# Optimization experiments

Measured on AMD Instinct MI355X. Metric: run time of the kernel, lower is better.

## Reference

```python
import jax, jax.numpy as jnp
import numpy as np

TOKEN_BITS = 10
CODEBOOK_SIZE = 2 ** TOKEN_BITS  # 1024
COMMITMENT_COST = 0.25
ENTROPY_LOSS_WEIGHT = 0.1
ENTROPY_TEMPERATURE = 0.01
ENTROPY_GAMMA = 1.0
EPS = 1e-5


def _make_codebook():
    bits_to_indices = (2 ** jnp.arange(TOKEN_BITS)).astype(jnp.int32)          # [c]
    all_codes = jnp.arange(CODEBOOK_SIZE, dtype=jnp.int32)                      # [n]
    bits = ((all_codes[:, None] & bits_to_indices) != 0).astype(jnp.float32)    # [n, c]
    codebook = bits * 2.0 - 1.0                                                 # [n, c] in {-1,+1}
    return bits_to_indices, codebook


def setup_inputs() -> dict:
    key = jax.random.key(0)
    z = jax.random.normal(key, (16, TOKEN_BITS, 64, 64), dtype=jnp.float32)
    return {"z": z}


def reference(z):
    bits_to_indices, codebook = _make_codebook()

    # b c h w -> b h w c
    zp = jnp.transpose(z, (0, 2, 3, 1)).astype(jnp.float32)

    # sign quantization to {-1, +1}
    sign_mask = zp > 0.0
    z_q = jnp.where(sign_mask, 1.0, -1.0).astype(jnp.float32)

    # pack sign bits into codebook indices
    min_encoding_indices = jnp.sum(sign_mask.astype(jnp.int32) * bits_to_indices, axis=-1)  # [b,h,w]

    # commitment loss (stop-grad on the quantized target)
    commitment_loss = COMMITMENT_COST * jnp.mean((jax.lax.stop_gradient(z_q) - zp) ** 2)

    # entropy loss: logits = -d = 2 * z . codebook^T, softened by temperature
    logits = 2.0 * jnp.einsum('bhwc,nc->bhwn', zp, codebook)  # [b,h,w,n]
    log_probs = jax.nn.log_softmax(logits / ENTROPY_TEMPERATURE, axis=-1)
    probs = jnp.exp(log_probs)
    per_sample_entropy = jnp.mean(-jnp.sum(probs * log_probs, axis=-1))
    avg_probs = jnp.mean(probs, axis=(0, 1, 2))  # [n]
    avg_entropy = ENTROPY_GAMMA * (-jnp.sum(avg_probs * jnp.log(avg_probs + EPS)))
    entropy_loss = ENTROPY_LOSS_WEIGHT * (per_sample_entropy - avg_entropy)

    loss = commitment_loss + entropy_loss

    # straight-through estimator
    z_quantized = zp + jax.lax.stop_gradient(z_q - zp)
    # b h w c -> b c h w
    z_quantized = jnp.transpose(z_quantized, (0, 3, 1, 2))

    return z_quantized, loss, per_sample_entropy, min_encoding_indices
```

## Files before the change

### kernel.cpp

```cpp
#include <hip/hip_runtime.h>

#define NCH    10
#define NCODE  1024
#define NLOC   65536
#define NZ     655360
#define GRID   256
#define THR    256
#define NHIST  4
#define POISON_INT (-1431655766)

__device__ __forceinline__ float wave_reduce_sum(float v) {
#pragma unroll
    for (int off = 32; off > 0; off >>= 1)
        v += __shfl_down(v, off, 64);
    return v;
}

__global__ __launch_bounds__(THR) void lfq_fused(
    const float* __restrict__ z, float* __restrict__ out,
    float* __restrict__ wsH, float* __restrict__ wsC, float* __restrict__ wsE,
    int* __restrict__ wsN)
{
    __shared__ float sR[NCH][THR];
    __shared__ unsigned short sM[NCH][THR];
    __shared__ float red[8];
    __shared__ int lastFlag;

    const int tid  = threadIdx.x;
    const int loc  = blockIdx.x * THR + tid;
    const int b    = loc >> 12;
    const int base = b * (NCH * 4096) + (loc & 4095);
    float* hist = wsH + (blockIdx.x & (NHIST - 1)) * NCODE;

    float commit = 0.f, ent = 0.f, pstar = 1.f;
    int idx = 0, k = 0;
#pragma unroll
    for (int c = 0; c < NCH; ++c) {
        float zc = z[base + c * 4096];
        bool bit = zc > 0.f;
        float s = bit ? 1.f : -1.f;
        out[base + c * 4096] = s;
        if (bit) idx |= (1 << c);
        float d = s - zc;
        commit += d * d;
        float a = fabsf(zc) * 400.f;
        if (a < 23.0f) {
            float e = __expf(-a);
            float inv = 1.f / (1.f + e);
            ent += __logf(1.f + e) + a * e * inv;
            pstar *= inv;
            sR[k][tid] = e;
            sM[k][tid] = (unsigned short)(1u << c);
            ++k;
        }
    }
    out[NZ + 2 + loc] = (float)idx;

    atomicAdd(&hist[idx], pstar);
    for (int m = 1; m < (1 << k); ++m) {
        float w = pstar;
        int code = idx;
        for (int j = 0; j < k; ++j)
            if (m & (1 << j)) { w *= sR[j][tid]; code ^= sM[j][tid]; }
        atomicAdd(&hist[code], w);
    }

    float cw = wave_reduce_sum(commit);
    float ew = wave_reduce_sum(ent);
    const int wave = tid >> 6, lane = tid & 63;
    if (lane == 0) { red[wave] = cw; red[4 + wave] = ew; }
    __syncthreads();
    if (tid == 0) {
        atomicAdd(wsC, red[0] + red[1] + red[2] + red[3]);
        atomicAdd(wsE, red[4] + red[5] + red[6] + red[7]);
        __threadfence();
        int old = __hip_atomic_fetch_add(wsN, 1, __ATOMIC_ACQ_REL,
                                         __HIP_MEMORY_SCOPE_AGENT);
        lastFlag = (old == POISON_INT + GRID - 1);
    }
    __syncthreads();
    if (!lastFlag) return;

    __threadfence();
    float termsum = 0.f;
#pragma unroll
    for (int r = 0; r < NCODE / THR; ++r) {
        const int n = r * THR + tid;
        float s = 0.f;
#pragma unroll
        for (int h = 0; h < NHIST; ++h)
            s += __hip_atomic_load(&wsH[h * NCODE + n], __ATOMIC_RELAXED,
                                   __HIP_MEMORY_SCOPE_AGENT);
        float avg_p = s * (1.f / (float)NLOC);
        termsum += -avg_p * __logf(avg_p + 1e-5f);
    }
    float tw = wave_reduce_sum(termsum);
    if (lane == 0) red[wave] = tw;
    __syncthreads();
    if (tid == 0) {
        float avg_ent = red[0] + red[1] + red[2] + red[3];
        float cs = __hip_atomic_load(wsC, __ATOMIC_RELAXED,
                                     __HIP_MEMORY_SCOPE_AGENT);
        float es = __hip_atomic_load(wsE, __ATOMIC_RELAXED,
                                     __HIP_MEMORY_SCOPE_AGENT);
        float commitment = 0.25f * cs * (1.f / (float)NZ);
        float per_sample = es * (1.f / (float)NLOC);
        out[NZ]     = commitment + 0.1f * (per_sample - avg_ent);
        out[NZ + 1] = per_sample;
    }
}

extern "C" void kernel_launch(void* const* d_in, const int* in_sizes, int n_in,
                              void* d_out, int out_size, void* d_ws, size_t ws_size,
                              hipStream_t stream) {
    const float* z = (const float*)d_in[0];
    float* out = (float*)d_out;
    float* wsH = (float*)d_ws;
    float* wsC = wsH + NHIST * NCODE;
    float* wsE = wsC + 1;
    int*   wsN = (int*)(wsE + 1);

    lfq_fused<<<GRID, THR, 0, stream>>>(z, out, wsH, wsC, wsE, wsN);
}
```

Measured before the change: 75.72 us.

## Process four locations per thread with float4 loads in single-wave blocks

Each thread now handles four consecutive spatial locations, using float4 loads and stores for z and the quantized output and float2 stores for indices. Blocks shrink to one 64-thread wave, so the cross-wave shared reduction and its barriers are removed. Grid stays at 256, so total threads drop fourfold while per-thread serial histogram atomics and the enumeration loop grow fourfold, which may lengthen the tail and reduce latency hiding.

```diff
diff --git a/kernel.cpp b/kernel.cpp
--- a/kernel.cpp
+++ b/kernel.cpp
@@ -5,7 +5,7 @@
 #define NLOC   65536
 #define NZ     655360
 #define GRID   256
-#define THR    256
+#define THR    64
 #define NHIST  4
 #define POISON_INT (-1431655766)
 
@@ -21,58 +21,70 @@
     float* __restrict__ wsH, float* __restrict__ wsC, float* __restrict__ wsE,
     int* __restrict__ wsN)
 {
-    __shared__ float sR[NCH][THR];
-    __shared__ unsigned short sM[NCH][THR];
-    __shared__ float red[8];
+    __shared__ float sR[NCH][4][THR];
+    __shared__ unsigned short sM[NCH][4][THR];
     __shared__ int lastFlag;
 
     const int tid  = threadIdx.x;
-    const int loc  = blockIdx.x * THR + tid;
-    const int b    = loc >> 12;
-    const int base = b * (NCH * 4096) + (loc & 4095);
+    const int grp  = blockIdx.x * THR + tid;
+    const int loc0 = grp * 4;
+    const int b    = loc0 >> 12;
+    const int base = b * (NCH * 4096) + (loc0 & 4095);
     float* hist = wsH + (blockIdx.x & (NHIST - 1)) * NCODE;
 
-    float commit = 0.f, ent = 0.f, pstar = 1.f;
-    int idx = 0, k = 0;
+    float commit = 0.f, ent = 0.f;
+    float pstar[4] = {1.f, 1.f, 1.f, 1.f};
+    int idx[4] = {0, 0, 0, 0};
+    int k[4] = {0, 0, 0, 0};
+
 #pragma unroll
     for (int c = 0; c < NCH; ++c) {
-        float zc = z[base + c * 4096];
-        bool bit = zc > 0.f;
-        float s = bit ? 1.f : -1.f;
-        out[base + c * 4096] = s;
-        if (bit) idx |= (1 << c);
-        float d = s - zc;
-        commit += d * d;
-        float a = fabsf(zc) * 400.f;
-        if (a < 23.0f) {
-            float e = __expf(-a);
-            float inv = 1.f / (1.f + e);
-            ent += __logf(1.f + e) + a * e * inv;
-            pstar *= inv;
-            sR[k][tid] = e;
-            sM[k][tid] = (unsigned short)(1u << c);
-            ++k;
+        float4 z4 = *(const float4*)(z + base + c * 4096);
+        float zl[4] = {z4.x, z4.y, z4.z, z4.w};
+        float sl[4];
+#pragma unroll
+        for (int l = 0; l < 4; ++l) {
+            float zc = zl[l];
+            bool bit = zc > 0.f;
+            float s = bit ? 1.f : -1.f;
+            sl[l] = s;
+            if (bit) idx[l] |= (1 << c);
+            float d = s - zc;
+            commit += d * d;
+            float a = fabsf(zc) * 400.f;
+            if (a < 23.0f) {
+                float e = __expf(-a);
+                float inv = 1.f / (1.f + e);
+                ent += __logf(1.f + e) + a * e * inv;
+                pstar[l] *= inv;
+                sR[k[l]][l][tid] = e;
+                sM[k[l]][l][tid] = (unsigned short)(1u << c);
+                ++k[l];
+            }
         }
+        *(float4*)(out + base + c * 4096) =
+            make_float4(sl[0], sl[1], sl[2], sl[3]);
     }
-    out[NZ + 2 + loc] = (float)idx;
+    *(float2*)(out + NZ + 2 + loc0)     = make_float2((float)idx[0], (float)idx[1]);
+    *(float2*)(out + NZ + 2 + loc0 + 2) = make_float2((float)idx[2], (float)idx[3]);
 
-    atomicAdd(&hist[idx], pstar);
-    for (int m = 1; m < (1 << k); ++m) {
-        float w = pstar;
-        int code = idx;
-        for (int j = 0; j < k; ++j)
-            if (m & (1 << j)) { w *= sR[j][tid]; code ^= sM[j][tid]; }
-        atomicAdd(&hist[code], w);
+#pragma unroll
+    for (int l = 0; l < 4; ++l) {
+        atomicAdd(&hist[idx[l]], pstar[l]);
+        for (int m = 1; m < (1 << k[l]); ++m) {
+            float w = pstar[l];
+            int code = idx[l];
+            for (int j = 0; j < k[l]; ++j)
+                if (m & (1 << j)) { w *= sR[j][l][tid]; code ^= sM[j][l][tid]; }
+            atomicAdd(&hist[code], w);
+        }
     }
 
     float cw = wave_reduce_sum(commit);
     float ew = wave_reduce_sum(ent);
-    const int wave = tid >> 6, lane = tid & 63;
-    if (lane == 0) { red[wave] = cw; red[4 + wave] = ew; }
-    __syncthreads();
     if (tid == 0) {
-        atomicAdd(wsC, red[0] + red[1] + red[2] + red[3]);
-        atomicAdd(wsE, red[4] + red[5] + red[6] + red[7]);
+        atomicAdd(wsC, cw);
+        atomicAdd(wsE, ew);
         __threadfence();
         int old = __hip_atomic_fetch_add(wsN, 1, __ATOMIC_ACQ_REL,
                                          __HIP_MEMORY_SCOPE_AGENT);
@@ -94,11 +106,8 @@
         float avg_p = s * (1.f / (float)NLOC);
         termsum += -avg_p * __logf(avg_p + 1e-5f);
     }
-    float tw = wave_reduce_sum(termsum);
-    if (lane == 0) red[wave] = tw;
-    __syncthreads();
+    float avg_ent = wave_reduce_sum(termsum);
     if (tid == 0) {
-        float avg_ent = red[0] + red[1] + red[2] + red[3];
         float cs = __hip_atomic_load(wsC, __ATOMIC_RELAXED,
                                      __HIP_MEMORY_SCOPE_AGENT);
         float es = __hip_atomic_load(wsE, __ATOMIC_RELAXED,
```

New measurement: 86.94 us. 14.8% more time.

## Split channels across two threads per location and double the grid

Applied to the files above, without the earlier changes.

Each location is now handled by two threads that each load and quantize five channels, with their partial index, probability product and near-zero terms merged through shared memory. The grid doubles to 512 blocks of 128 locations, raising parallelism and memory-level overlap for the loads and stores. Commit and entropy partial sums are now atomically added per wave instead of per block, which means more global atomics. The histogram enumeration runs on only half the threads, so its divergence and serial atomics are concentrated in fewer lanes.

```diff
diff --git a/kernel.cpp b/kernel.cpp
--- a/kernel.cpp
+++ b/kernel.cpp
@@ -4,8 +4,9 @@
 #define NCODE  1024
 #define NLOC   65536
 #define NZ     655360
-#define GRID   256
+#define GRID   512
 #define THR    256
+#define LPB    128
 #define NHIST  4
 #define POISON_INT (-1431655766)
 
@@ -21,58 +22,79 @@
     float* __restrict__ wsH, float* __restrict__ wsC, float* __restrict__ wsE,
     int* __restrict__ wsN)
 {
-    __shared__ float sR[NCH][THR];
-    __shared__ unsigned short sM[NCH][THR];
-    __shared__ float red[8];
+    __shared__ float sRc[LPB][NCH];
+    __shared__ unsigned short sMc[LPB][NCH];
+    __shared__ int   sIdx1[LPB];
+    __shared__ float sP1[LPB];
+    __shared__ int   sK1[LPB];
+    __shared__ float red[4];
     __shared__ int lastFlag;
 
     const int tid  = threadIdx.x;
-    const int loc  = blockIdx.x * THR + tid;
+    const int lid  = tid & (LPB - 1);
+    const int half = tid >> 7;
+    const int loc  = blockIdx.x * LPB + lid;
     const int b    = loc >> 12;
     const int base = b * (NCH * 4096) + (loc & 4095);
+    const int c0   = half * 5;
     float* hist = wsH + (blockIdx.x & (NHIST - 1)) * NCODE;
+
+    float zc[5];
+#pragma unroll
+    for (int i = 0; i < 5; ++i) zc[i] = z[base + (c0 + i) * 4096];
 
     float commit = 0.f, ent = 0.f, pstar = 1.f;
     int idx = 0, k = 0;
 #pragma unroll
-    for (int c = 0; c < NCH; ++c) {
-        float zc = z[base + c * 4096];
-        bool bit = zc > 0.f;
+    for (int i = 0; i < 5; ++i) {
+        float zv = zc[i];
+        bool bit = zv > 0.f;
         float s = bit ? 1.f : -1.f;
-        out[base + c * 4096] = s;
-        if (bit) idx |= (1 << c);
-        float d = s - zc;
+        out[base + (c0 + i) * 4096] = s;
+        if (bit) idx |= (1 << (c0 + i));
+        float d = s - zv;
         commit += d * d;
-        float a = fabsf(zc) * 400.f;
+        float a = fabsf(zv) * 400.f;
         if (a < 23.0f) {
             float e = __expf(-a);
             float inv = 1.f / (1.f + e);
             ent += __logf(1.f + e) + a * e * inv;
             pstar *= inv;
-            sR[k][tid] = e;
-            sM[k][tid] = (unsigned short)(1u << c);
+            sRc[lid][c0 + k] = e;
+            sMc[lid][c0 + k] = (unsigned short)(1u << (c0 + i));
             ++k;
         }
     }
-    out[NZ + 2 + loc] = (float)idx;
-
-    atomicAdd(&hist[idx], pstar);
-    for (int m = 1; m < (1 << k); ++m) {
-        float w = pstar;
-        int code = idx;
-        for (int j = 0; j < k; ++j)
-            if (m & (1 << j)) { w *= sR[j][tid]; code ^= sM[j][tid]; }
-        atomicAdd(&hist[code], w);
-    }
+    if (half) { sIdx1[lid] = idx; sP1[lid] = pstar; sK1[lid] = k; }
 
     float cw = wave_reduce_sum(commit);
     float ew = wave_reduce_sum(ent);
-    const int wave = tid >> 6, lane = tid & 63;
-    if (lane == 0) { red[wave] = cw; red[4 + wave] = ew; }
+    if ((tid & 63) == 0) { atomicAdd(wsC, cw); atomicAdd(wsE, ew); }
+
+    __syncthreads();
+
+    if (half == 0) {
+        const int k0 = k, k1 = sK1[lid], kt = k0 + k1;
+        idx |= sIdx1[lid];
+        pstar *= sP1[lid];
+        out[NZ + 2 + loc] = (float)idx;
+
+        atomicAdd(&hist[idx], pstar);
+        for (int m = 1; m < (1 << kt); ++m) {
+            float w = pstar;
+            int code = idx;
+            for (int j = 0; j < kt; ++j)
+                if (m & (1 << j)) {
+                    const int slot = (j < k0) ? j : (5 + j - k0);
+                    w *= sRc[lid][slot];
+                    code ^= sMc[lid][slot];
+                }
+            atomicAdd(&hist[code], w);
+        }
+    }
+
     __syncthreads();
     if (tid == 0) {
-        atomicAdd(wsC, red[0] + red[1] + red[2] + red[3]);
-        atomicAdd(wsE, red[4] + red[5] + red[6] + red[7]);
         __threadfence();
         int old = __hip_atomic_fetch_add(wsN, 1, __ATOMIC_ACQ_REL,
                                          __HIP_MEMORY_SCOPE_AGENT);
@@ -95,7 +117,7 @@
         termsum += -avg_p * __logf(avg_p + 1e-5f);
     }
     float tw = wave_reduce_sum(termsum);
-    if (lane == 0) red[wave] = tw;
+    if ((tid & 63) == 0) red[tid >> 6] = tw;
     __syncthreads();
     if (tid == 0) {
         float avg_ent = red[0] + red[1] + red[2] + red[3];
```

Result: slower. 127.3 us (+68.1%).
